# Optimization experiments

Measured on AMD Instinct MI355X. Metric: run time of the kernel, lower is better.

The kernel has to match this reference:

```python
import jax, jax.numpy as jnp
import numpy as np

D_MODEL = 1024
D_STATE = 128
D_CONV = 4
EXPAND = 2
HEADDIM = 64
D_INNER = EXPAND * D_MODEL          # 2048
NHEADS = D_INNER // HEADDIM         # 32
NGROUPS = 1
CONV_DIM = D_INNER + 2 * NGROUPS * D_STATE            # 2304
D_IN_PROJ = 2 * D_INNER + 2 * NGROUPS * D_STATE + NHEADS  # 4384
NUM_CLASS = 48
BATCH = 2
SEQLEN = 512


def setup_inputs() -> dict:
    key = jax.random.key(0)
    ks = jax.random.split(key, 8)
    s = 0.02
    inputs = jax.random.normal(ks[0], (BATCH, SEQLEN, D_MODEL), jnp.float32)
    W_in = jax.random.normal(ks[1], (D_MODEL, D_IN_PROJ), jnp.float32) * s
    conv_w = jax.random.normal(ks[2], (CONV_DIM, D_CONV), jnp.float32) * 0.2
    conv_b = jnp.zeros((CONV_DIM,), jnp.float32)
    # dt_bias = inverse-softplus of dt sampled in [1e-3, 0.1] (mamba init)
    dt = jnp.exp(jax.random.uniform(ks[3], (NHEADS,), jnp.float32) * (np.log(0.1) - np.log(1e-3)) + np.log(1e-3))
    dt_bias = dt + jnp.log(-jnp.expm1(-dt))
    A_log = jnp.log(jax.random.uniform(ks[4], (NHEADS,), jnp.float32, 1.0, 16.0))
    D = jnp.ones((NHEADS,), jnp.float32)
    norm_w = jnp.ones((D_INNER,), jnp.float32)
    W_out = jax.random.normal(ks[5], (D_INNER, D_MODEL), jnp.float32) * s
    W_cls = jax.random.normal(ks[6], (D_INNER, NUM_CLASS), jnp.float32) * s
    b_cls = jnp.zeros((NUM_CLASS,), jnp.float32)
    return {"inputs": inputs, "W_in": W_in, "conv_w": conv_w, "conv_b": conv_b,
            "dt_bias": dt_bias, "A_log": A_log, "D": D, "norm_w": norm_w,
            "W_out": W_out, "W_cls": W_cls, "b_cls": b_cls}


def _forward(inputs, W_in, conv_w, conv_b, dt_bias, A_log, D, norm_w, W_out, W_cls, b_cls):
    B, L, _ = inputs.shape
    zxbcdt = inputs @ W_in                                     # (B,L,4384)
    z, xBC, dt = jnp.split(zxbcdt, [D_INNER, D_INNER + CONV_DIM], axis=-1)
    dt = jax.nn.softplus(dt + dt_bias)                         # (B,L,H)
    # causal depthwise conv over time on (x,B,C)
    xBC_t = jnp.pad(jnp.transpose(xBC, (0, 2, 1)), ((0, 0), (0, 0), (D_CONV - 1, 0)))
    xBC_c = jax.lax.conv_general_dilated(xBC_t, conv_w[:, None, :], (1,), 'VALID',
                                         feature_group_count=CONV_DIM)
    xBC = jax.nn.silu(jnp.transpose(xBC_c, (0, 2, 1)) + conv_b)
    x, Bm, Cm = jnp.split(xBC, [D_INNER, D_INNER + D_STATE], axis=-1)
    x = x.reshape(B, L, NHEADS, HEADDIM)
    A = -jnp.exp(A_log)                                        # (H,)
    dA = jnp.exp(dt * A)                                       # (B,L,H)

    def step(state, inp):
        # state: (B,H,P,N) -- selective SSM recurrence (chunk_size=1 path)
        x_t, B_t, C_t, dt_t, dA_t = inp
        state = state * dA_t[:, :, None, None] + jnp.einsum('bhp,bn,bh->bhpn', x_t, B_t, dt_t)
        y_t = jnp.einsum('bhpn,bn->bhp', state, C_t)
        return state, y_t

    state0 = jnp.zeros((B, NHEADS, HEADDIM, D_STATE), inputs.dtype)
    xs = (jnp.transpose(x, (1, 0, 2, 3)), jnp.transpose(Bm, (1, 0, 2)),
          jnp.transpose(Cm, (1, 0, 2)), jnp.transpose(dt, (1, 0, 2)),
          jnp.transpose(dA, (1, 0, 2)))
    _, ys = jax.lax.scan(step, state0, xs)                     # ys: (L,B,H,P)
    y = jnp.transpose(ys, (1, 0, 2, 3)) + D[None, None, :, None] * x
    y = y.reshape(B, L, D_INNER)
    # gated RMSNorm: rmsnorm(y * silu(z)) * weight
    y = y * jax.nn.silu(z)
    y = y * jax.lax.rsqrt(jnp.mean(y * y, axis=-1, keepdims=True) + 1e-5) * norm_w
    # hidden_states (d_inner=2048) go through the per-timestep classifier
    preds = y @ W_cls + b_cls                                  # (B,L,num_class)
    return preds


def reference(inputs, W_in, conv_w, conv_b, dt_bias, A_log, D, norm_w, W_out, W_cls, b_cls):
    return _forward(inputs, W_in, conv_w, conv_b, dt_bias, A_log, D, norm_w, W_out, W_cls, b_cls)
```

## Files before the change

### kernel.cpp

```cpp
#include <hip/hip_runtime.h>
#include <hip/hip_bf16.h>
#include <cstdint>

#define BATCH 2
#define SEQLEN 512
#define BL (BATCH*SEQLEN)
#define DMODEL 1024
#define DINNER 2048
#define NHEADS 32
#define HEADDIM 64
#define DSTATE 128
#define CONVDIM 2304
#define DINPROJ 4384
#define NPROJPAD 4480
#define NCLS 48
#define QC 64
#define NCH 8

typedef short bf16x8 __attribute__((ext_vector_type(8)));
typedef float f32x4  __attribute__((ext_vector_type(4)));
typedef unsigned int u32;
typedef const __attribute__((address_space(1))) u32 gu32;
typedef __attribute__((address_space(3))) u32 lu32;

static __device__ __forceinline__ void gl16(const void* g, void* l) {
    __builtin_amdgcn_global_load_lds((gu32*)g, (lu32*)l, 16, 0, 0);
}

static __device__ __forceinline__ unsigned short f2bf(float f) {
    unsigned u = __float_as_uint(f);
    unsigned r = (u + 0x7FFFu + ((u >> 16) & 1u)) >> 16;
    return (unsigned short)r;
}
static __device__ __forceinline__ float bf2f(unsigned short u) {
    return __uint_as_float(((unsigned)u) << 16);
}

__global__ __launch_bounds__(256) void k_cvt_a(const float* __restrict__ in,
                                               unsigned short* __restrict__ out) {
    int i = (blockIdx.x * 256 + threadIdx.x) * 4;
    float4 v = *(const float4*)(in + i);
    ushort4 o;
    o.x = f2bf(v.x); o.y = f2bf(v.y); o.z = f2bf(v.z); o.w = f2bf(v.w);
    *(ushort4*)(out + i) = o;
}

__global__ __launch_bounds__(256) void k_transpose_w(const float* __restrict__ W,
                                                     unsigned short* __restrict__ Wt) {
    __shared__ float tile[32][33];
    int n0 = blockIdx.x * 32;
    int k0 = blockIdx.y * 32;
    int tx = threadIdx.x & 31;
    int ty = threadIdx.x >> 5;
#pragma unroll
    for (int i = 0; i < 4; ++i) {
        int k = k0 + ty + i * 8;
        tile[ty + i * 8][tx] = W[(size_t)k * DINPROJ + n0 + tx];
    }
    __syncthreads();
#pragma unroll
    for (int i = 0; i < 4; ++i) {
        int n = n0 + ty + i * 8;
        Wt[(size_t)n * DMODEL + k0 + tx] = f2bf(tile[tx][ty + i * 8]);
    }
}

__global__ __launch_bounds__(256) void k_prep_cls(const float* __restrict__ W,
                                                  const float* __restrict__ bcls,
                                                  unsigned short* __restrict__ Wt,
                                                  float* __restrict__ out) {
    int bid = blockIdx.x;
    if (bid < 192) {
        int i = bid * 256 + threadIdx.x;
        out[i] = bcls[i % NCLS];
    } else {
        int n = bid - 192;
        for (int k = threadIdx.x; k < DINNER; k += 256)
            Wt[(size_t)n * DINNER + k] = f2bf(W[(size_t)k * NCLS + n]);
    }
}

__global__ __launch_bounds__(256) void k_gemm_in(const unsigned short* __restrict__ A,
                                                 const unsigned short* __restrict__ Bt,
                                                 unsigned short* __restrict__ C) {
    __shared__ unsigned short As[2 * 4096];
    __shared__ unsigned short Bs[2 * 4096];
    const int tid  = threadIdx.x;
    const int m0   = blockIdx.y * 128;
    const int n0   = blockIdx.x * 128;
    const int w    = tid >> 6;
    const int lane = tid & 63;
    const int wm   = w >> 1, wn = w & 1;
    const int fr   = lane & 15, fq = lane >> 4;
    const int srow = w * 16 + (lane >> 2);
    const int skg  = (lane & 3) * 8;
    const unsigned short* gA0 = A  + (size_t)(m0 + srow) * DMODEL + skg;
    const unsigned short* gA1 = gA0 + (size_t)64 * DMODEL;
    const unsigned short* gB0 = Bt + (size_t)(n0 + srow) * DMODEL + skg;
    const unsigned short* gB1 = gB0 + (size_t)64 * DMODEL;

    f32x4 acc[4][4] = {};
    for (int k0 = 0; k0 < DMODEL; k0 += 64) {
        __syncthreads();
#pragma unroll
        for (int hh = 0; hh < 2; ++hh) {
            int kg = k0 + hh * 32;
            gl16(gA0 + kg, As + hh * 4096 + w * 512);
            gl16(gA1 + kg, As + hh * 4096 + 2048 + w * 512);
            gl16(gB0 + kg, Bs + hh * 4096 + w * 512);
            gl16(gB1 + kg, Bs + hh * 4096 + 2048 + w * 512);
        }
        __syncthreads();
#pragma unroll
        for (int hh = 0; hh < 2; ++hh) {
            bf16x8 af[4], bf[4];
#pragma unroll
            for (int mt = 0; mt < 4; ++mt)
                af[mt] = *(const bf16x8*)(&As[hh * 4096 + (wm * 64 + mt * 16 + fr) * 32 + fq * 8]);
#pragma unroll
            for (int nt = 0; nt < 4; ++nt)
                bf[nt] = *(const bf16x8*)(&Bs[hh * 4096 + (wn * 64 + nt * 16 + fr) * 32 + fq * 8]);
#pragma unroll
            for (int mt = 0; mt < 4; ++mt)
#pragma unroll
                for (int nt = 0; nt < 4; ++nt)
                    acc[mt][nt] = __builtin_amdgcn_mfma_f32_16x16x32_bf16(af[mt], bf[nt], acc[mt][nt], 0, 0, 0);
        }
    }
#pragma unroll
    for (int mt = 0; mt < 4; ++mt) {
#pragma unroll
        for (int nt = 0; nt < 4; ++nt) {
            int col = n0 + wn * 64 + nt * 16 + fr;
            if (col < DINPROJ) {
#pragma unroll
                for (int r = 0; r < 4; ++r) {
                    int row = m0 + wm * 64 + mt * 16 + fq * 4 + r;
                    C[(size_t)row * DINPROJ + col] = f2bf(acc[mt][nt][r]);
                }
            }
        }
    }
}

__global__ __launch_bounds__(256) void k_conv_dt(const unsigned short* __restrict__ zx,
                                                 const float* __restrict__ conv_w,
                                                 const float* __restrict__ conv_b,
                                                 const float* __restrict__ dt_bias,
                                                 float* __restrict__ xbc,
                                                 float* __restrict__ dtb) {
    int row = blockIdx.y;
    int c   = blockIdx.x * 256 + threadIdx.x;
    int b = row >> 9, l = row & 511;
    if (c < CONVDIM) {
        float acc = conv_b[c];
#pragma unroll
        for (int j = 0; j < 4; ++j) {
            int ls = l - 3 + j;
            float v = (ls >= 0) ? bf2f(zx[((size_t)(b * SEQLEN + ls)) * DINPROJ + DINNER + c]) : 0.f;
            acc += v * conv_w[c * 4 + j];
        }
        float s = acc / (1.f + expf(-acc));
        xbc[(size_t)row * CONVDIM + c] = s;
    } else if (c < CONVDIM + NHEADS) {
        int h = c - CONVDIM;
        float raw = bf2f(zx[(size_t)row * DINPROJ + (DINNER + CONVDIM) + h]) + dt_bias[h];
        float dt = (raw > 20.f) ? raw : log1pf(expf(raw));
        dtb[row * NHEADS + h] = dt;
    }
}

__global__ __launch_bounds__(256) void k_chunk(const float* __restrict__ xbc,
                                               const float* __restrict__ dtb,
                                               const float* __restrict__ A_log,
                                               const float* __restrict__ Dvec,
                                               float* __restrict__ yb,
                                               float* __restrict__ Sc_g,
                                               float* __restrict__ lam_g,
                                               float* __restrict__ esc_g) {
    const int gid = blockIdx.x;
    const int c = gid & 7;
    const int h = (gid >> 3) & 31;
    const int b = gid >> 8;
    const int row0 = b * SEQLEN + c * QC;

    __shared__ float cumS[QC], wS[QC], dtS[QC];
    __shared__ unsigned short Xt[QC][72];
    __shared__ unsigned short Bs[QC][136];
    __shared__ unsigned short BtW[DSTATE][72];
    __shared__ unsigned short Cs[QC][136];
    __shared__ unsigned short Gs[QC][72];

    const int tid = threadIdx.x;
    if (tid < 64) {
        float dtv = dtb[(size_t)(row0 + tid) * NHEADS + h];
        float nA = -expf(A_log[h]);
        float x = dtv * nA;
#pragma unroll
        for (int off = 1; off < 64; off <<= 1) {
            float v = __shfl_up(x, off, 64);
            if (tid >= off) x += v;
        }
        float cumTot = __shfl(x, 63, 64);
        cumS[tid] = x;
        dtS[tid] = dtv;
        wS[tid] = expf(cumTot - x) * dtv;
        esc_g[(size_t)gid * QC + tid] = expf(x);
        if (tid == 0) lam_g[gid] = expf(cumTot);
    }
    __syncthreads();

    {
        int row = tid >> 2;
        int g = tid & 3;
        const float* rp = xbc + (size_t)(row0 + row) * CONVDIM;
        float wrow = wS[row];
#pragma unroll
        for (int i = 0; i < 4; ++i) {
            float4 v = *(const float4*)(rp + h * HEADDIM + g * 16 + i * 4);
            int p = g * 16 + i * 4;
            Xt[p + 0][row] = f2bf(v.x);
            Xt[p + 1][row] = f2bf(v.y);
            Xt[p + 2][row] = f2bf(v.z);
            Xt[p + 3][row] = f2bf(v.w);
        }
#pragma unroll
        for (int i = 0; i < 8; ++i) {
            int n = g * 32 + i * 4;
            float4 v = *(const float4*)(rp + DINNER + n);
            ushort4 u;
            u.x = f2bf(v.x); u.y = f2bf(v.y); u.z = f2bf(v.z); u.w = f2bf(v.w);
            *(ushort4*)(&Bs[row][n]) = u;
            BtW[n + 0][row] = f2bf(v.x * wrow);
            BtW[n + 1][row] = f2bf(v.y * wrow);
            BtW[n + 2][row] = f2bf(v.z * wrow);
            BtW[n + 3][row] = f2bf(v.w * wrow);
        }
#pragma unroll
        for (int i = 0; i < 8; ++i) {
            int n = g * 32 + i * 4;
            float4 v = *(const float4*)(rp + DINNER + DSTATE + n);
            ushort4 u;
            u.x = f2bf(v.x); u.y = f2bf(v.y); u.z = f2bf(v.z); u.w = f2bf(v.w);
            *(ushort4*)(&Cs[row][n]) = u;
        }
    }
    __syncthreads();

    const int w = tid >> 6, lane = tid & 63;
    const int fr = lane & 15, fq = lane >> 4, fk = (lane >> 4) * 8;

    f32x4 accG[4] = {};
#pragma unroll
    for (int kk = 0; kk < 4; ++kk) {
        bf16x8 a = *(const bf16x8*)(&Cs[w * 16 + fr][kk * 32 + fk]);
#pragma unroll
        for (int nt = 0; nt < 4; ++nt) {
            bf16x8 bb = *(const bf16x8*)(&Bs[nt * 16 + fr][kk * 32 + fk]);
            accG[nt] = __builtin_amdgcn_mfma_f32_16x16x32_bf16(a, bb, accG[nt], 0, 0, 0);
        }
    }
#pragma unroll
    for (int nt = 0; nt < 4; ++nt) {
        int s = nt * 16 + fr;
        float cs = cumS[s], dts = dtS[s];
#pragma unroll
        for (int r = 0; r < 4; ++r) {
            int t = w * 16 + fq * 4 + r;
            float val = (s <= t) ? accG[nt][r] * expf(cumS[t] - cs) * dts : 0.f;
            Gs[t][s] = f2bf(val);
        }
    }
    __syncthreads();

    f32x4 accY[4] = {};
#pragma unroll
    for (int kk = 0; kk < 2; ++kk) {
        bf16x8 a = *(const bf16x8*)(&Gs[w * 16 + fr][kk * 32 + fk]);
#pragma unroll
        for (int pt = 0; pt < 4; ++pt) {
            bf16x8 bb = *(const bf16x8*)(&Xt[pt * 16 + fr][kk * 32 + fk]);
            accY[pt] = __builtin_amdgcn_mfma_f32_16x16x32_bf16(a, bb, accY[pt], 0, 0, 0);
        }
    }
    f32x4 accS[8] = {};
#pragma unroll
    for (int kk = 0; kk < 2; ++kk) {
        bf16x8 a = *(const bf16x8*)(&Xt[w * 16 + fr][kk * 32 + fk]);
#pragma unroll
        for (int nt = 0; nt < 8; ++nt) {
            bf16x8 bb = *(const bf16x8*)(&BtW[nt * 16 + fr][kk * 32 + fk]);
            accS[nt] = __builtin_amdgcn_mfma_f32_16x16x32_bf16(a, bb, accS[nt], 0, 0, 0);
        }
    }
    float Dh = Dvec[h];
#pragma unroll
    for (int pt = 0; pt < 4; ++pt) {
        int p = pt * 16 + fr;
#pragma unroll
        for (int r = 0; r < 4; ++r) {
            int t = w * 16 + fq * 4 + r;
            float xv = xbc[(size_t)(row0 + t) * CONVDIM + h * HEADDIM + p];
            yb[(size_t)(row0 + t) * DINNER + h * HEADDIM + p] = accY[pt][r] + Dh * xv;
        }
    }
    float* scp = Sc_g + (size_t)gid * (HEADDIM * DSTATE);
#pragma unroll
    for (int nt = 0; nt < 8; ++nt) {
        int n = nt * 16 + fr;
#pragma unroll
        for (int r = 0; r < 4; ++r) {
            int p = w * 16 + fq * 4 + r;
            scp[p * DSTATE + n] = accS[nt][r];
        }
    }
}

__global__ __launch_bounds__(256) void k_chain(const float* __restrict__ Sc_g,
                                               const float* __restrict__ lam_g,
                                               unsigned short* __restrict__ Sin_bf) {
    int bh = blockIdx.x >> 2;
    int sl = blockIdx.x & 3;
    int tid = threadIdx.x;
    float s[8];
#pragma unroll
    for (int i = 0; i < 8; ++i) s[i] = 0.f;
    for (int c = 0; c < NCH; ++c) {
        size_t base = (size_t)(bh * NCH + c) * (HEADDIM * DSTATE) + sl * 2048 + tid * 8;
#pragma unroll
        for (int j = 0; j < 8; j += 4) {
            ushort4 u;
            u.x = f2bf(s[j + 0]); u.y = f2bf(s[j + 1]);
            u.z = f2bf(s[j + 2]); u.w = f2bf(s[j + 3]);
            *(ushort4*)(Sin_bf + base + j) = u;
        }
        float lam = lam_g[bh * NCH + c];
#pragma unroll
        for (int j = 0; j < 8; j += 4) {
            float4 v = *(const float4*)(Sc_g + base + j);
            s[j + 0] = s[j + 0] * lam + v.x;
            s[j + 1] = s[j + 1] * lam + v.y;
            s[j + 2] = s[j + 2] * lam + v.z;
            s[j + 3] = s[j + 3] * lam + v.w;
        }
    }
}

__global__ __launch_bounds__(256) void k_cross(const float* __restrict__ xbc,
                                               const float* __restrict__ esc_g,
                                               const unsigned short* __restrict__ Sin_bf,
                                               float* __restrict__ yb) {
    const int gid = blockIdx.x;
    const int c = gid & 7;
    const int h = (gid >> 3) & 31;
    const int b = gid >> 8;
    const int row0 = b * SEQLEN + c * QC;
    __shared__ unsigned short Ct[QC][136];
    __shared__ unsigned short Ss[QC][136];
    const int tid = threadIdx.x;
    {
        int row = tid >> 2, g = tid & 3;
        const float* rp = xbc + (size_t)(row0 + row) * CONVDIM + DINNER + DSTATE;
        float esc = esc_g[(size_t)gid * QC + row];
#pragma unroll
        for (int i = 0; i < 8; ++i) {
            int n = g * 32 + i * 4;
            float4 v = *(const float4*)(rp + n);
            ushort4 u;
            u.x = f2bf(v.x * esc); u.y = f2bf(v.y * esc);
            u.z = f2bf(v.z * esc); u.w = f2bf(v.w * esc);
            *(ushort4*)(&Ct[row][n]) = u;
        }
        const uint4* sp = (const uint4*)(Sin_bf + (size_t)gid * (HEADDIM * DSTATE));
#pragma unroll
        for (int i = 0; i < 4; ++i) {
            uint4 v = sp[row * 16 + g * 4 + i];
            *(uint4*)(&Ss[row][g * 32 + i * 8]) = v;
        }
    }
    __syncthreads();
    const int w = tid >> 6, lane = tid & 63;
    const int fr = lane & 15, fq = lane >> 4, fk = (lane >> 4) * 8;
    f32x4 acc[4] = {};
#pragma unroll
    for (int kk = 0; kk < 4; ++kk) {
        bf16x8 a = *(const bf16x8*)(&Ct[w * 16 + fr][kk * 32 + fk]);
#pragma unroll
        for (int pt = 0; pt < 4; ++pt) {
            bf16x8 bb = *(const bf16x8*)(&Ss[pt * 16 + fr][kk * 32 + fk]);
            acc[pt] = __builtin_amdgcn_mfma_f32_16x16x32_bf16(a, bb, acc[pt], 0, 0, 0);
        }
    }
#pragma unroll
    for (int pt = 0; pt < 4; ++pt) {
        int p = pt * 16 + fr;
#pragma unroll
        for (int r = 0; r < 4; ++r) {
            int t = w * 16 + fq * 4 + r;
            size_t yi = (size_t)(row0 + t) * DINNER + h * HEADDIM + p;
            yb[yi] += acc[pt][r];
        }
    }
}

__global__ __launch_bounds__(256) void k_gate_norm(const unsigned short* __restrict__ zx,
                                                   const float* __restrict__ nw,
                                                   const float* __restrict__ y,
                                                   unsigned short* __restrict__ Gbf) {
    int row = blockIdx.x;
    int tid = threadIdx.x;
    const unsigned short* zrow = zx + (size_t)row * DINPROJ;
    const float* yr = y + (size_t)row * DINNER;
    float g[8];
    float ss = 0.f;
#pragma unroll
    for (int i = 0; i < 2; ++i) {
        int c = tid * 4 + i * 1024;
        float4 yv = *(const float4*)(yr + c);
        ushort4 zv = *(const ushort4*)(zrow + c);
        float zs[4] = {bf2f(zv.x), bf2f(zv.y), bf2f(zv.z), bf2f(zv.w)};
        float ys[4] = {yv.x, yv.y, yv.z, yv.w};
#pragma unroll
        for (int k = 0; k < 4; ++k) {
            float sil = zs[k] / (1.f + expf(-zs[k]));
            float gg = ys[k] * sil;
            g[i * 4 + k] = gg;
            ss += gg * gg;
        }
    }
#pragma unroll
    for (int off = 32; off >= 1; off >>= 1) ss += __shfl_xor(ss, off, 64);
    __shared__ float wsum[4];
    if ((tid & 63) == 0) wsum[tid >> 6] = ss;
    __syncthreads();
    float tot = wsum[0] + wsum[1] + wsum[2] + wsum[3];
    float scale = rsqrtf(tot / (float)DINNER + 1e-5f);
#pragma unroll
    for (int i = 0; i < 2; ++i) {
        int c = tid * 4 + i * 1024;
        float4 nv = *(const float4*)(nw + c);
        ushort4 o;
        o.x = f2bf(g[i * 4 + 0] * scale * nv.x);
        o.y = f2bf(g[i * 4 + 1] * scale * nv.y);
        o.z = f2bf(g[i * 4 + 2] * scale * nv.z);
        o.w = f2bf(g[i * 4 + 3] * scale * nv.w);
        *(ushort4*)(Gbf + (size_t)row * DINNER + c) = o;
    }
}

__global__ __launch_bounds__(256) void k_cls_mfma(const unsigned short* __restrict__ G,
                                                  const unsigned short* __restrict__ Wt,
                                                  float* __restrict__ out) {
    __shared__ unsigned short Gs[64][72];
    __shared__ unsigned short Ws[48][72];
    const int m0  = blockIdx.x * 64;
    const int k00 = blockIdx.y * 256;
    const int tid = threadIdx.x;
    const int w = tid >> 6, lane = tid & 63;
    const int fr = lane & 15, fq = lane >> 4, fk = fq * 8;
    f32x4 acc[3] = {};
    for (int ks = 0; ks < 4; ++ks) {
        int k0 = k00 + ks * 64;
        __syncthreads();
        {
            int row = tid >> 2, seg = (tid & 3) * 16;
            const unsigned short* gp = G + (size_t)(m0 + row) * DINNER + k0 + seg;
            *(uint4*)(&Gs[row][seg])     = *(const uint4*)(gp);
            *(uint4*)(&Gs[row][seg + 8]) = *(const uint4*)(gp + 8);
        }
        if (tid < 192) {
            int row = tid >> 2, seg = (tid & 3) * 16;
            const unsigned short* wp = Wt + (size_t)row * DINNER + k0 + seg;
            *(uint4*)(&Ws[row][seg])     = *(const uint4*)(wp);
            *(uint4*)(&Ws[row][seg + 8]) = *(const uint4*)(wp + 8);
        }
        __syncthreads();
#pragma unroll
        for (int kk = 0; kk < 2; ++kk) {
            bf16x8 a = *(const bf16x8*)(&Gs[w * 16 + fr][kk * 32 + fk]);
#pragma unroll
            for (int nt = 0; nt < 3; ++nt) {
                bf16x8 bb = *(const bf16x8*)(&Ws[nt * 16 + fr][kk * 32 + fk]);
                acc[nt] = __builtin_amdgcn_mfma_f32_16x16x32_bf16(a, bb, acc[nt], 0, 0, 0);
            }
        }
    }
#pragma unroll
    for (int nt = 0; nt < 3; ++nt) {
        int col = nt * 16 + fr;
#pragma unroll
        for (int r = 0; r < 4; ++r) {
            int row = m0 + w * 16 + fq * 4 + r;
            atomicAdd(&out[(size_t)row * NCLS + col], acc[nt][r]);
        }
    }
}

extern "C" void kernel_launch(void* const* d_in, const int* in_sizes, int n_in,
                              void* d_out, int out_size, void* d_ws, size_t ws_size,
                              hipStream_t stream) {
    const float* inputs  = (const float*)d_in[0];
    const float* W_in    = (const float*)d_in[1];
    const float* conv_w  = (const float*)d_in[2];
    const float* conv_b  = (const float*)d_in[3];
    const float* dt_bias = (const float*)d_in[4];
    const float* A_log   = (const float*)d_in[5];
    const float* Dvec    = (const float*)d_in[6];
    const float* norm_w  = (const float*)d_in[7];
    const float* W_cls   = (const float*)d_in[9];
    const float* b_cls   = (const float*)d_in[10];
    float* out = (float*)d_out;

    float* ws   = (float*)d_ws;
    unsigned short* zxb = (unsigned short*)ws;
    float* xbc  = ws   + (size_t)BL * DINPROJ / 2 + 512;
    float* dtb  = xbc  + (size_t)BL * CONVDIM;
    float* yb   = dtb  + (size_t)BL * NHEADS;
    float* Sc_g = yb   + (size_t)BL * DINNER;
    float* lam_g= Sc_g + (size_t)BATCH * NHEADS * NCH * HEADDIM * DSTATE;
    float* esc_g= lam_g+ (size_t)BATCH * NHEADS * NCH;
    unsigned short* Sin_bf = (unsigned short*)(esc_g + (size_t)BATCH * NHEADS * NCH * QC);
    unsigned short* abf    = Sin_bf + (size_t)BATCH * NHEADS * NCH * HEADDIM * DSTATE;
    unsigned short* wtbf   = abf + (size_t)BL * DMODEL;
    unsigned short* wclsbf = wtbf + (size_t)NPROJPAD * DMODEL;
    unsigned short* Gbf    = (unsigned short*)Sc_g;

    k_cvt_a<<<dim3(BL * DMODEL / (256 * 4)), dim3(256), 0, stream>>>(inputs, abf);
    k_transpose_w<<<dim3(DINPROJ / 32, DMODEL / 32), dim3(256), 0, stream>>>(W_in, wtbf);
    k_prep_cls<<<dim3(240), dim3(256), 0, stream>>>(W_cls, b_cls, wclsbf, out);
    k_gemm_in<<<dim3(NPROJPAD / 128, BL / 128), dim3(256), 0, stream>>>(abf, wtbf, zxb);
    k_conv_dt<<<dim3(10, BL), dim3(256), 0, stream>>>(zxb, conv_w, conv_b, dt_bias, xbc, dtb);
    k_chunk<<<dim3(BATCH * NHEADS * NCH), dim3(256), 0, stream>>>(xbc, dtb, A_log, Dvec,
                                                                  yb, Sc_g, lam_g, esc_g);
    k_chain<<<dim3(BATCH * NHEADS * 4), dim3(256), 0, stream>>>(Sc_g, lam_g, Sin_bf);
    k_cross<<<dim3(BATCH * NHEADS * NCH), dim3(256), 0, stream>>>(xbc, esc_g, Sin_bf, yb);
    k_gate_norm<<<dim3(BL), dim3(256), 0, stream>>>(zxb, norm_w, yb, Gbf);
    k_cls_mfma<<<dim3(BL / 64, 8), dim3(256), 0, stream>>>(Gbf, wclsbf, out);
}
```

Measured before the change: 171.4 us.

## Fuse prep kernels, store intermediates in bf16, fuse gated-norm with classifier

Merges the input-conversion, W_in transpose and W_cls transpose into one launch, and drops the bias prefill of the output. Stores the y buffer and the per-chunk states in bf16 instead of fp32 to halve their memory traffic. Fuses the gated RMSNorm with the classifier GEMM: each block normalises 16 rows in shared memory, splits K across waves, reduces partials in LDS and adds the bias, removing the Gbf round trip and the atomics. The costs are extra bf16 rounding on y and the chunk states, and a per-block read of the classifier weights straight from global memory.

Result: no change. 174.0 us (+1.6%).

```diff
diff --git a/kernel.cpp b/kernel.cpp
--- a/kernel.cpp
+++ b/kernel.cpp
@@ -36,47 +36,41 @@
     return __uint_as_float(((unsigned)u) << 16);
 }
 
-__global__ __launch_bounds__(256) void k_cvt_a(const float* __restrict__ in,
-                                               unsigned short* __restrict__ out) {
-    int i = (blockIdx.x * 256 + threadIdx.x) * 4;
-    float4 v = *(const float4*)(in + i);
-    ushort4 o;
-    o.x = f2bf(v.x); o.y = f2bf(v.y); o.z = f2bf(v.z); o.w = f2bf(v.w);
-    *(ushort4*)(out + i) = o;
-}
-
-__global__ __launch_bounds__(256) void k_transpose_w(const float* __restrict__ W,
-                                                     unsigned short* __restrict__ Wt) {
+__global__ __launch_bounds__(256) void k_prep(const float* __restrict__ in,
+                                              unsigned short* __restrict__ abf,
+                                              const float* __restrict__ W,
+                                              unsigned short* __restrict__ Wt,
+                                              const float* __restrict__ Wcls,
+                                              unsigned short* __restrict__ Wtc) {
     __shared__ float tile[32][33];
-    int n0 = blockIdx.x * 32;
-    int k0 = blockIdx.y * 32;
-    int tx = threadIdx.x & 31;
-    int ty = threadIdx.x >> 5;
-#pragma unroll
-    for (int i = 0; i < 4; ++i) {
-        int k = k0 + ty + i * 8;
-        tile[ty + i * 8][tx] = W[(size_t)k * DINPROJ + n0 + tx];
-    }
-    __syncthreads();
-#pragma unroll
-    for (int i = 0; i < 4; ++i) {
-        int n = n0 + ty + i * 8;
-        Wt[(size_t)n * DMODEL + k0 + tx] = f2bf(tile[tx][ty + i * 8]);
-    }
-}
-
-__global__ __launch_bounds__(256) void k_prep_cls(const float* __restrict__ W,
-                                                  const float* __restrict__ bcls,
-                                                  unsigned short* __restrict__ Wt,
-                                                  float* __restrict__ out) {
     int bid = blockIdx.x;
-    if (bid < 192) {
-        int i = bid * 256 + threadIdx.x;
-        out[i] = bcls[i % NCLS];
+    int tid = threadIdx.x;
+    if (bid < 1024) {
+        int i = (bid * 256 + tid) * 4;
+        float4 v = *(const float4*)(in + i);
+        ushort4 o;
+        o.x = f2bf(v.x); o.y = f2bf(v.y); o.z = f2bf(v.z); o.w = f2bf(v.w);
+        *(ushort4*)(abf + i) = o;
+    } else if (bid < 1024 + 4384) {
+        int t = bid - 1024;
+        int n0 = (t % 137) * 32;
+        int k0 = (t / 137) * 32;
+        int tx = tid & 31, ty = tid >> 5;
+#pragma unroll
+        for (int i = 0; i < 4; ++i) {
+            int k = k0 + ty + i * 8;
+            tile[ty + i * 8][tx] = W[(size_t)k * DINPROJ + n0 + tx];
+        }
+        __syncthreads();
+#pragma unroll
+        for (int i = 0; i < 4; ++i) {
+            int n = n0 + ty + i * 8;
+            Wt[(size_t)n * DMODEL + k0 + tx] = f2bf(tile[tx][ty + i * 8]);
+        }
     } else {
-        int n = bid - 192;
-        for (int k = threadIdx.x; k < DINNER; k += 256)
-            Wt[(size_t)n * DINNER + k] = f2bf(W[(size_t)k * NCLS + n]);
+        int n = bid - (1024 + 4384);
+        for (int k = tid; k < DINNER; k += 256)
+            Wtc[(size_t)n * DINNER + k] = f2bf(Wcls[(size_t)k * NCLS + n]);
     }
 }
 
@@ -113,18 +107,18 @@
         __syncthreads();
 #pragma unroll
         for (int hh = 0; hh < 2; ++hh) {
-            bf16x8 af[4], bf[4];
+            bf16x8 af[4], bfr[4];
 #pragma unroll
             for (int mt = 0; mt < 4; ++mt)
                 af[mt] = *(const bf16x8*)(&As[hh * 4096 + (wm * 64 + mt * 16 + fr) * 32 + fq * 8]);
 #pragma unroll
             for (int nt = 0; nt < 4; ++nt)
-                bf[nt] = *(const bf16x8*)(&Bs[hh * 4096 + (wn * 64 + nt * 16 + fr) * 32 + fq * 8]);
+                bfr[nt] = *(const bf16x8*)(&Bs[hh * 4096 + (wn * 64 + nt * 16 + fr) * 32 + fq * 8]);
 #pragma unroll
             for (int mt = 0; mt < 4; ++mt)
 #pragma unroll
                 for (int nt = 0; nt < 4; ++nt)
-                    acc[mt][nt] = __builtin_amdgcn_mfma_f32_16x16x32_bf16(af[mt], bf[nt], acc[mt][nt], 0, 0, 0);
+                    acc[mt][nt] = __builtin_amdgcn_mfma_f32_16x16x32_bf16(af[mt], bfr[nt], acc[mt][nt], 0, 0, 0);
         }
     }
 #pragma unroll
@@ -174,15 +168,15 @@
                                                const float* __restrict__ dtb,
                                                const float* __restrict__ A_log,
                                                const float* __restrict__ Dvec,
-                                               float* __restrict__ yb,
-                                               float* __restrict__ Sc_g,
+                                               unsigned short* __restrict__ yb,
+                                               unsigned short* __restrict__ Sc_bf,
                                                float* __restrict__ lam_g,
                                                float* __restrict__ esc_g) {
     const int gid = blockIdx.x;
-    const int c = gid & 7;
+    const int cq = gid & 7;
     const int h = (gid >> 3) & 31;
     const int b = gid >> 8;
-    const int row0 = b * SEQLEN + c * QC;
+    const int row0 = b * SEQLEN + cq * QC;
 
     __shared__ float cumS[QC], wS[QC], dtS[QC];
     __shared__ unsigned short Xt[QC][72];
@@ -301,22 +295,22 @@
         for (int r = 0; r < 4; ++r) {
             int t = w * 16 + fq * 4 + r;
             float xv = xbc[(size_t)(row0 + t) * CONVDIM + h * HEADDIM + p];
-            yb[(size_t)(row0 + t) * DINNER + h * HEADDIM + p] = accY[pt][r] + Dh * xv;
-        }
-    }
-    float* scp = Sc_g + (size_t)gid * (HEADDIM * DSTATE);
+            yb[(size_t)(row0 + t) * DINNER + h * HEADDIM + p] = f2bf(accY[pt][r] + Dh * xv);
+        }
+    }
+    unsigned short* scp = Sc_bf + (size_t)gid * (HEADDIM * DSTATE);
 #pragma unroll
     for (int nt = 0; nt < 8; ++nt) {
         int n = nt * 16 + fr;
 #pragma unroll
         for (int r = 0; r < 4; ++r) {
             int p = w * 16 + fq * 4 + r;
-            scp[p * DSTATE + n] = accS[nt][r];
-        }
-    }
-}
-
-__global__ __launch_bounds__(256) void k_chain(const float* __restrict__ Sc_g,
+            scp[p * DSTATE + n] = f2bf(accS[nt][r]);
+        }
+    }
+}
+
+__global__ __launch_bounds__(256) void k_chain(const unsigned short* __restrict__ Sc_bf,
                                                const float* __restrict__ lam_g,
                                                unsigned short* __restrict__ Sin_bf) {
     int bh = blockIdx.x >> 2;
@@ -327,34 +321,34 @@
     for (int i = 0; i < 8; ++i) s[i] = 0.f;
     for (int c = 0; c < NCH; ++c) {
         size_t base = (size_t)(bh * NCH + c) * (HEADDIM * DSTATE) + sl * 2048 + tid * 8;
-#pragma unroll
-        for (int j = 0; j < 8; j += 4) {
-            ushort4 u;
-            u.x = f2bf(s[j + 0]); u.y = f2bf(s[j + 1]);
-            u.z = f2bf(s[j + 2]); u.w = f2bf(s[j + 3]);
-            *(ushort4*)(Sin_bf + base + j) = u;
-        }
+        ushort4 o0, o1;
+        o0.x = f2bf(s[0]); o0.y = f2bf(s[1]); o0.z = f2bf(s[2]); o0.w = f2bf(s[3]);
+        o1.x = f2bf(s[4]); o1.y = f2bf(s[5]); o1.z = f2bf(s[6]); o1.w = f2bf(s[7]);
+        *(ushort4*)(Sin_bf + base) = o0;
+        *(ushort4*)(Sin_bf + base + 4) = o1;
         float lam = lam_g[bh * NCH + c];
-#pragma unroll
-        for (int j = 0; j < 8; j += 4) {
-            float4 v = *(const float4*)(Sc_g + base + j);
-            s[j + 0] = s[j + 0] * lam + v.x;
-            s[j + 1] = s[j + 1] * lam + v.y;
-            s[j + 2] = s[j + 2] * lam + v.z;
-            s[j + 3] = s[j + 3] * lam + v.w;
-        }
+        ushort4 v0 = *(const ushort4*)(Sc_bf + base);
+        ushort4 v1 = *(const ushort4*)(Sc_bf + base + 4);
+        s[0] = s[0] * lam + bf2f(v0.x);
+        s[1] = s[1] * lam + bf2f(v0.y);
+        s[2] = s[2] * lam + bf2f(v0.z);
+        s[3] = s[3] * lam + bf2f(v0.w);
+        s[4] = s[4] * lam + bf2f(v1.x);
+        s[5] = s[5] * lam + bf2f(v1.y);
+        s[6] = s[6] * lam + bf2f(v1.z);
+        s[7] = s[7] * lam + bf2f(v1.w);
     }
 }
 
 __global__ __launch_bounds__(256) void k_cross(const float* __restrict__ xbc,
                                                const float* __restrict__ esc_g,
                                                const unsigned short* __restrict__ Sin_bf,
-                                               float* __restrict__ yb) {
+                                               unsigned short* __restrict__ yb) {
     const int gid = blockIdx.x;
-    const int c = gid & 7;
+    const int cq = gid & 7;
     const int h = (gid >> 3) & 31;
     const int b = gid >> 8;
-    const int row0 = b * SEQLEN + c * QC;
+    const int row0 = b * SEQLEN + cq * QC;
     __shared__ unsigned short Ct[QC][136];
     __shared__ unsigned short Ss[QC][136];
     const int tid = threadIdx.x;
@@ -398,100 +392,115 @@
         for (int r = 0; r < 4; ++r) {
             int t = w * 16 + fq * 4 + r;
             size_t yi = (size_t)(row0 + t) * DINNER + h * HEADDIM + p;
-            yb[yi] += acc[pt][r];
-        }
-    }
-}
-
-__global__ __launch_bounds__(256) void k_gate_norm(const unsigned short* __restrict__ zx,
-                                                   const float* __restrict__ nw,
-                                                   const float* __restrict__ y,
-                                                   unsigned short* __restrict__ Gbf) {
-    int row = blockIdx.x;
-    int tid = threadIdx.x;
-    const unsigned short* zrow = zx + (size_t)row * DINPROJ;
-    const float* yr = y + (size_t)row * DINNER;
-    float g[8];
-    float ss = 0.f;
-#pragma unroll
-    for (int i = 0; i < 2; ++i) {
-        int c = tid * 4 + i * 1024;
-        float4 yv = *(const float4*)(yr + c);
-        ushort4 zv = *(const ushort4*)(zrow + c);
-        float zs[4] = {bf2f(zv.x), bf2f(zv.y), bf2f(zv.z), bf2f(zv.w)};
-        float ys[4] = {yv.x, yv.y, yv.z, yv.w};
-#pragma unroll
-        for (int k = 0; k < 4; ++k) {
-            float sil = zs[k] / (1.f + expf(-zs[k]));
-            float gg = ys[k] * sil;
-            g[i * 4 + k] = gg;
-            ss += gg * gg;
-        }
-    }
-#pragma unroll
-    for (int off = 32; off >= 1; off >>= 1) ss += __shfl_xor(ss, off, 64);
-    __shared__ float wsum[4];
-    if ((tid & 63) == 0) wsum[tid >> 6] = ss;
-    __syncthreads();
-    float tot = wsum[0] + wsum[1] + wsum[2] + wsum[3];
-    float scale = rsqrtf(tot / (float)DINNER + 1e-5f);
-#pragma unroll
-    for (int i = 0; i < 2; ++i) {
-        int c = tid * 4 + i * 1024;
-        float4 nv = *(const float4*)(nw + c);
-        ushort4 o;
-        o.x = f2bf(g[i * 4 + 0] * scale * nv.x);
-        o.y = f2bf(g[i * 4 + 1] * scale * nv.y);
-        o.z = f2bf(g[i * 4 + 2] * scale * nv.z);
-        o.w = f2bf(g[i * 4 + 3] * scale * nv.w);
-        *(ushort4*)(Gbf + (size_t)row * DINNER + c) = o;
-    }
-}
-
-__global__ __launch_bounds__(256) void k_cls_mfma(const unsigned short* __restrict__ G,
-                                                  const unsigned short* __restrict__ Wt,
-                                                  float* __restrict__ out) {
-    __shared__ unsigned short Gs[64][72];
-    __shared__ unsigned short Ws[48][72];
-    const int m0  = blockIdx.x * 64;
-    const int k00 = blockIdx.y * 256;
+            yb[yi] = f2bf(bf2f(yb[yi]) + acc[pt][r]);
+        }
+    }
+}
+
+__global__ __launch_bounds__(256) void k_gn_cls(const unsigned short* __restrict__ zx,
+                                                const unsigned short* __restrict__ yb,
+                                                const float* __restrict__ nw,
+                                                const unsigned short* __restrict__ Wt,
+                                                const float* __restrict__ bcls,
+                                                float* __restrict__ out) {
+    __shared__ unsigned short Gs[16][2048];
+    __shared__ float scaleS[16];
+    __shared__ float Rs[3][4][256];
+    const int m0 = blockIdx.x * 16;
     const int tid = threadIdx.x;
     const int w = tid >> 6, lane = tid & 63;
-    const int fr = lane & 15, fq = lane >> 4, fk = fq * 8;
+
+#pragma unroll
+    for (int i = 0; i < 4; ++i) {
+        int rl = w * 4 + i;
+        int row = m0 + rl;
+        const unsigned short* yr = yb + (size_t)row * DINNER;
+        const unsigned short* zr = zx + (size_t)row * DINPROJ;
+        float gv[32];
+        float ss = 0.f;
+#pragma unroll
+        for (int i2 = 0; i2 < 4; ++i2) {
+            int k = i2 * 512 + lane * 8;
+            ushort4 ya = *(const ushort4*)(yr + k);
+            ushort4 ybq = *(const ushort4*)(yr + k + 4);
+            ushort4 za = *(const ushort4*)(zr + k);
+            ushort4 zbq = *(const ushort4*)(zr + k + 4);
+            float ys[8] = {bf2f(ya.x), bf2f(ya.y), bf2f(ya.z), bf2f(ya.w),
+                           bf2f(ybq.x), bf2f(ybq.y), bf2f(ybq.z), bf2f(ybq.w)};
+            float zs[8] = {bf2f(za.x), bf2f(za.y), bf2f(za.z), bf2f(za.w),
+                           bf2f(zbq.x), bf2f(zbq.y), bf2f(zbq.z), bf2f(zbq.w)};
+#pragma unroll
+            for (int j = 0; j < 8; ++j) {
+                float sil = zs[j] / (1.f + expf(-zs[j]));
+                float gg = ys[j] * sil;
+                gv[i2 * 8 + j] = gg;
+                ss += gg * gg;
+            }
+        }
+#pragma unroll
+        for (int off = 32; off >= 1; off >>= 1) ss += __shfl_xor(ss, off, 64);
+        if (lane == 0) scaleS[rl] = rsqrtf(ss / (float)DINNER + 1e-5f);
+#pragma unroll
+        for (int i2 = 0; i2 < 4; ++i2) {
+            int k = i2 * 512 + lane * 8;
+            ushort4 u0, u1;
+            u0.x = f2bf(gv[i2 * 8 + 0]); u0.y = f2bf(gv[i2 * 8 + 1]);
+            u0.z = f2bf(gv[i2 * 8 + 2]); u0.w = f2bf(gv[i2 * 8 + 3]);
+            u1.x = f2bf(gv[i2 * 8 + 4]); u1.y = f2bf(gv[i2 * 8 + 5]);
+            u1.z = f2bf(gv[i2 * 8 + 6]); u1.w = f2bf(gv[i2 * 8 + 7]);
+            *(ushort4*)(&Gs[rl][k]) = u0;
+            *(ushort4*)(&Gs[rl][k + 4]) = u1;
+        }
+    }
+    __syncthreads();
+    {
+        int k0 = tid * 8;
+        float4 n0 = *(const float4*)(nw + k0);
+        float4 n1 = *(const float4*)(nw + k0 + 4);
+        float nv[8] = {n0.x, n0.y, n0.z, n0.w, n1.x, n1.y, n1.z, n1.w};
+#pragma unroll
+        for (int r = 0; r < 16; ++r) {
+            float sc = scaleS[r];
+            ushort4 a0 = *(const ushort4*)(&Gs[r][k0]);
+            ushort4 a1 = *(const ushort4*)(&Gs[r][k0 + 4]);
+            ushort4 o0, o1;
+            o0.x = f2bf(bf2f(a0.x) * sc * nv[0]); o0.y = f2bf(bf2f(a0.y) * sc * nv[1]);
+            o0.z = f2bf(bf2f(a0.z) * sc * nv[2]); o0.w = f2bf(bf2f(a0.w) * sc * nv[3]);
+            o1.x = f2bf(bf2f(a1.x) * sc * nv[4]); o1.y = f2bf(bf2f(a1.y) * sc * nv[5]);
+            o1.z = f2bf(bf2f(a1.z) * sc * nv[6]); o1.w = f2bf(bf2f(a1.w) * sc * nv[7]);
+            *(ushort4*)(&Gs[r][k0]) = o0;
+            *(ushort4*)(&Gs[r][k0 + 4]) = o1;
+        }
+    }
+    __syncthreads();
+    const int fr = lane & 15, fq = lane >> 4;
     f32x4 acc[3] = {};
-    for (int ks = 0; ks < 4; ++ks) {
-        int k0 = k00 + ks * 64;
-        __syncthreads();
-        {
-            int row = tid >> 2, seg = (tid & 3) * 16;
-            const unsigned short* gp = G + (size_t)(m0 + row) * DINNER + k0 + seg;
-            *(uint4*)(&Gs[row][seg])     = *(const uint4*)(gp);
-            *(uint4*)(&Gs[row][seg + 8]) = *(const uint4*)(gp + 8);
-        }
-        if (tid < 192) {
-            int row = tid >> 2, seg = (tid & 3) * 16;
-            const unsigned short* wp = Wt + (size_t)row * DINNER + k0 + seg;
-            *(uint4*)(&Ws[row][seg])     = *(const uint4*)(wp);
-            *(uint4*)(&Ws[row][seg + 8]) = *(const uint4*)(wp + 8);
-        }
-        __syncthreads();
-#pragma unroll
-        for (int kk = 0; kk < 2; ++kk) {
-            bf16x8 a = *(const bf16x8*)(&Gs[w * 16 + fr][kk * 32 + fk]);
-#pragma unroll
-            for (int nt = 0; nt < 3; ++nt) {
-                bf16x8 bb = *(const bf16x8*)(&Ws[nt * 16 + fr][kk * 32 + fk]);
-                acc[nt] = __builtin_amdgcn_mfma_f32_16x16x32_bf16(a, bb, acc[nt], 0, 0, 0);
+    const int kbase = w * 512;
+    for (int ks = 0; ks < 16; ++ks) {
+        int k0 = kbase + ks * 32;
+        bf16x8 a = *(const bf16x8*)(&Gs[fr][k0 + fq * 8]);
+#pragma unroll
+        for (int nt = 0; nt < 3; ++nt) {
+            bf16x8 bb = *(const bf16x8*)(Wt + (size_t)(nt * 16 + fr) * DINNER + k0 + fq * 8);
+            acc[nt] = __builtin_amdgcn_mfma_f32_16x16x32_bf16(a, bb, acc[nt], 0, 0, 0);
+        }
+    }
+#pragma unroll
+    for (int nt = 0; nt < 3; ++nt)
+        *(f32x4*)(&Rs[nt][w][lane * 4]) = acc[nt];
+    __syncthreads();
+    if (tid < 64) {
+#pragma unroll
+        for (int nt = 0; nt < 3; ++nt) {
+            int col = nt * 16 + (lane & 15);
+            float bb = bcls[col];
+#pragma unroll
+            for (int j = 0; j < 4; ++j) {
+                float s = Rs[nt][0][lane * 4 + j] + Rs[nt][1][lane * 4 + j]
+                        + Rs[nt][2][lane * 4 + j] + Rs[nt][3][lane * 4 + j];
+                int row = m0 + (lane >> 4) * 4 + j;
+                out[(size_t)row * NCLS + col] = s + bb;
             }
-        }
-    }
-#pragma unroll
-    for (int nt = 0; nt < 3; ++nt) {
-        int col = nt * 16 + fr;
-#pragma unroll
-        for (int r = 0; r < 4; ++r) {
-            int row = m0 + w * 16 + fq * 4 + r;
-            atomicAdd(&out[(size_t)row * NCLS + col], acc[nt][r]);
         }
     }
 }
@@ -511,29 +520,26 @@
     const float* b_cls   = (const float*)d_in[10];
     float* out = (float*)d_out;
 
-    float* ws   = (float*)d_ws;
+    float* ws = (float*)d_ws;
     unsigned short* zxb = (unsigned short*)ws;
-    float* xbc  = ws   + (size_t)BL * DINPROJ / 2 + 512;
-    float* dtb  = xbc  + (size_t)BL * CONVDIM;
-    float* yb   = dtb  + (size_t)BL * NHEADS;
-    float* Sc_g = yb   + (size_t)BL * DINNER;
-    float* lam_g= Sc_g + (size_t)BATCH * NHEADS * NCH * HEADDIM * DSTATE;
-    float* esc_g= lam_g+ (size_t)BATCH * NHEADS * NCH;
-    unsigned short* Sin_bf = (unsigned short*)(esc_g + (size_t)BATCH * NHEADS * NCH * QC);
-    unsigned short* abf    = Sin_bf + (size_t)BATCH * NHEADS * NCH * HEADDIM * DSTATE;
+    float* xbc   = ws + (size_t)BL * DINPROJ / 2;
+    float* dtb   = xbc + (size_t)BL * CONVDIM;
+    float* lam_g = dtb + (size_t)BL * NHEADS;
+    float* esc_g = lam_g + 512;
+    unsigned short* yb     = (unsigned short*)(esc_g + 512 * QC);
+    unsigned short* Sc_bf  = yb + (size_t)BL * DINNER;
+    unsigned short* Sin_bf = Sc_bf + (size_t)512 * HEADDIM * DSTATE;
+    unsigned short* abf    = Sin_bf + (size_t)512 * HEADDIM * DSTATE;
     unsigned short* wtbf   = abf + (size_t)BL * DMODEL;
     unsigned short* wclsbf = wtbf + (size_t)NPROJPAD * DMODEL;
-    unsigned short* Gbf    = (unsigned short*)Sc_g;
-
-    k_cvt_a<<<dim3(BL * DMODEL / (256 * 4)), dim3(256), 0, stream>>>(inputs, abf);
-    k_transpose_w<<<dim3(DINPROJ / 32, DMODEL / 32), dim3(256), 0, stream>>>(W_in, wtbf);
-    k_prep_cls<<<dim3(240), dim3(256), 0, stream>>>(W_cls, b_cls, wclsbf, out);
+
+    k_prep<<<dim3(1024 + 4384 + 48), dim3(256), 0, stream>>>(inputs, abf, W_in, wtbf,
+                                                             W_cls, wclsbf);
     k_gemm_in<<<dim3(NPROJPAD / 128, BL / 128), dim3(256), 0, stream>>>(abf, wtbf, zxb);
     k_conv_dt<<<dim3(10, BL), dim3(256), 0, stream>>>(zxb, conv_w, conv_b, dt_bias, xbc, dtb);
     k_chunk<<<dim3(BATCH * NHEADS * NCH), dim3(256), 0, stream>>>(xbc, dtb, A_log, Dvec,
-                                                                  yb, Sc_g, lam_g, esc_g);
-    k_chain<<<dim3(BATCH * NHEADS * 4), dim3(256), 0, stream>>>(Sc_g, lam_g, Sin_bf);
+                                                                  yb, Sc_bf, lam_g, esc_g);
+    k_chain<<<dim3(BATCH * NHEADS * 4), dim3(256), 0, stream>>>(Sc_bf, lam_g, Sin_bf);
     k_cross<<<dim3(BATCH * NHEADS * NCH), dim3(256), 0, stream>>>(xbc, esc_g, Sin_bf, yb);
-    k_gate_norm<<<dim3(BL), dim3(256), 0, stream>>>(zxb, norm_w, yb, Gbf);
-    k_cls_mfma<<<dim3(BL / 64, 8), dim3(256), 0, stream>>>(Gbf, wclsbf, out);
-}
+    k_gn_cls<<<dim3(BL / 16), dim3(256), 0, stream>>>(zxb, yb, norm_w, wclsbf, b_cls, out);
+}
```
